# Performance work log

Measured on AMD Instinct MI355X. Metric: run time of the kernel, lower is better.

The kernel has to match this reference:

```python
import jax, jax.numpy as jnp
import numpy as np

EPS = 1e-5
DN = ('NCHW', 'OIHW', 'NCHW')


def ternarize(w):
    """Ternary Weight Network quantization with straight-through estimator.
    delta = 0.7 * mean|w|; alpha = mean of |w| over kept entries.
    """
    aw = jnp.abs(w)
    delta = 0.7 * aw.mean()
    mask = (aw > delta).astype(w.dtype)
    alpha = (aw * mask).sum() / jnp.maximum(mask.sum(), 1.0)
    q = alpha * jnp.sign(w) * mask
    return w + jax.lax.stop_gradient(q - w)


def bn(y, g, b, m, v):
    scale = (g / jnp.sqrt(v + EPS))[None, :, None, None]
    shift = (b - m * g / jnp.sqrt(v + EPS))[None, :, None, None]
    return y * scale + shift


def relu6(y):
    return jnp.clip(y, 0.0, 6.0)


def conv(x, w, stride=1, padding='VALID'):
    return jax.lax.conv_general_dilated(
        x, w, window_strides=(stride, stride), padding=padding,
        dimension_numbers=DN)


def setup_inputs() -> dict:
    key = jax.random.key(0)
    ks = jax.random.split(key, 16)
    inp, oup, expand = 32, 32, 6
    hidden = inp * expand  # 192
    B, H, W = 16, 112, 112
    d = {}
    d['x'] = jax.random.normal(ks[0], (B, inp, H, W), dtype=jnp.float32)
    # 1x1 expand conv
    d['w1'] = jax.random.normal(ks[1], (hidden, inp, 1, 1), dtype=jnp.float32) * 0.1
    d['g1'] = 1.0 + 0.1 * jax.random.normal(ks[2], (hidden,), dtype=jnp.float32)
    d['b1'] = 0.1 * jax.random.normal(ks[3], (hidden,), dtype=jnp.float32)
    d['m1'] = 0.1 * jax.random.normal(ks[4], (hidden,), dtype=jnp.float32)
    d['v1'] = jax.random.uniform(ks[5], (hidden,), minval=0.5, maxval=1.5, dtype=jnp.float32)
    # 3x3 dense conv (no groups in the source -> dense, not depthwise)
    d['w2'] = jax.random.normal(ks[6], (hidden, hidden, 3, 3), dtype=jnp.float32) * 0.05
    d['g2'] = 1.0 + 0.1 * jax.random.normal(ks[7], (hidden,), dtype=jnp.float32)
    d['b2'] = 0.1 * jax.random.normal(ks[8], (hidden,), dtype=jnp.float32)
    d['m2'] = 0.1 * jax.random.normal(ks[9], (hidden,), dtype=jnp.float32)
    d['v2'] = jax.random.uniform(ks[10], (hidden,), minval=0.5, maxval=1.5, dtype=jnp.float32)
    # 1x1 project conv
    d['w3'] = jax.random.normal(ks[11], (oup, hidden, 1, 1), dtype=jnp.float32) * 0.1
    d['g3'] = 1.0 + 0.1 * jax.random.normal(ks[12], (oup,), dtype=jnp.float32)
    d['b3'] = 0.1 * jax.random.normal(ks[13], (oup,), dtype=jnp.float32)
    d['m3'] = 0.1 * jax.random.normal(ks[14], (oup,), dtype=jnp.float32)
    d['v3'] = jax.random.uniform(ks[15], (oup,), minval=0.5, maxval=1.5, dtype=jnp.float32)
    return d


def reference(x, w1, g1, b1, m1, v1, w2, g2, b2, m2, v2, w3, g3, b3, m3, v3):
    # expand: 1x1 ternary conv -> BN -> ReLU6
    h = relu6(bn(conv(x, ternarize(w1)), g1, b1, m1, v1))
    # 3x3 ternary conv (stride=1, padding=1) -> BN -> ReLU6
    h = relu6(bn(conv(h, ternarize(w2), stride=1, padding=((1, 1), (1, 1))), g2, b2, m2, v2))
    # project: 1x1 ternary conv -> BN (no activation)
    h = bn(conv(h, ternarize(w3)), g3, b3, m3, v3)
    # residual connection (stride==1 and inp==oup)
    return x + h
```

## Files before the change

### kernel.cpp

```cpp
#include <hip/hip_runtime.h>


typedef __bf16 bf16x8 __attribute__((ext_vector_type(8)));
typedef __bf16 bf16x4 __attribute__((ext_vector_type(4)));
typedef float  f32x4  __attribute__((ext_vector_type(4)));

#define EPSBN 1e-5f

__device__ __forceinline__ void glds16(const void* g, void* l) {
  __builtin_amdgcn_global_load_lds(
      (const __attribute__((address_space(1))) void*)g,
      (__attribute__((address_space(3))) void*)l, 16, 0, 0);
}

__device__ __forceinline__ __bf16 tern(float w, float delta) {
  float aw = fabsf(w);
  float q = (aw > delta) ? ((w > 0.0f) ? 1.0f : -1.0f) : 0.0f;
  return (__bf16)q;
}


__global__ void stats_pass1(const float* __restrict__ w1, const float* __restrict__ w2,
                            const float* __restrict__ w3, double* __restrict__ pa) {
  __shared__ double red[256];
  int b = blockIdx.x, tid = threadIdx.x;
  int tix = b >> 5, slice = b & 31;
  const float* w = (tix == 0) ? w1 : (tix == 1) ? w2 : w3;
  int len = (tix == 1) ? 331776 : 6144;
  int per = len >> 5;
  int start = slice * per, end = start + per;
  double s = 0.0;
  for (int i = start + tid; i < end; i += 256) s += (double)fabsf(w[i]);
  red[tid] = s; __syncthreads();
  for (int off = 128; off > 0; off >>= 1) {
    if (tid < off) red[tid] += red[tid + off];
    __syncthreads();
  }
  if (tid == 0) pa[b] = red[0];
}

__global__ void stats_pass2(const float* __restrict__ w1, const float* __restrict__ w2,
                            const float* __restrict__ w3, const double* __restrict__ pa,
                            double* __restrict__ ps2, double* __restrict__ pc2) {
  __shared__ double red[256];
  int b = blockIdx.x, tid = threadIdx.x;
  int tix = b >> 5, slice = b & 31;
  const float* w = (tix == 0) ? w1 : (tix == 1) ? w2 : w3;
  int len = (tix == 1) ? 331776 : 6144;
  double tot = 0.0;
  for (int k = 0; k < 32; ++k) tot += pa[tix * 32 + k];
  float delta = 0.7f * (float)(tot / (double)len);
  int per = len >> 5;
  int start = slice * per, end = start + per;
  double s2 = 0.0, c2 = 0.0;
  for (int i = start + tid; i < end; i += 256) {
    float aw = fabsf(w[i]);
    if (aw > delta) { s2 += (double)aw; c2 += 1.0; }
  }
  red[tid] = s2; __syncthreads();
  for (int off = 128; off > 0; off >>= 1) {
    if (tid < off) red[tid] += red[tid + off];
    __syncthreads();
  }
  if (tid == 0) ps2[b] = red[0];
  __syncthreads();
  red[tid] = c2; __syncthreads();
  for (int off = 128; off > 0; off >>= 1) {
    if (tid < off) red[tid] += red[tid + off];
    __syncthreads();
  }
  if (tid == 0) pc2[b] = red[0];
}

__global__ void stats_pass3(const double* __restrict__ pa, const double* __restrict__ ps2,
                            const double* __restrict__ pc2, float* __restrict__ stats) {
  int tix = blockIdx.x;
  if (threadIdx.x != 0) return;
  double tot = 0.0, s2 = 0.0, c2 = 0.0;
  for (int k = 0; k < 32; ++k) {
    tot += pa[tix * 32 + k];
    s2  += ps2[tix * 32 + k];
    c2  += pc2[tix * 32 + k];
  }
  int len = (tix == 1) ? 331776 : 6144;
  stats[tix * 2]     = 0.7f * (float)(tot / (double)len);
  stats[tix * 2 + 1] = (float)(s2 / fmax(c2, 1.0));
}

__global__ void pack_kernel(
    const float* __restrict__ w1, const float* __restrict__ w2, const float* __restrict__ w3,
    const float* __restrict__ g1, const float* __restrict__ b1, const float* __restrict__ m1, const float* __restrict__ v1,
    const float* __restrict__ g2, const float* __restrict__ b2, const float* __restrict__ m2, const float* __restrict__ v2,
    const float* __restrict__ g3, const float* __restrict__ b3, const float* __restrict__ m3, const float* __restrict__ v3,
    const float* __restrict__ stats,
    __bf16* __restrict__ w1p, __bf16* __restrict__ w2p, __bf16* __restrict__ w3p,
    float* __restrict__ sc1, float* __restrict__ sh1,
    float* __restrict__ sc2, float* __restrict__ sh2,
    float* __restrict__ sc3, float* __restrict__ sh3) {
  int idx = blockIdx.x * 256 + threadIdx.x;
  if (idx < 331776) {
    float delta2 = stats[2];
    int c = idx / 6144, rem = idx - c * 6144;
    int co = rem >> 5, r5 = rem & 31;
    int cp = r5 >> 3, lo = r5 & 7;
    int tap = c / 6, cb = c - tap * 6;
    int ci = ((cp ^ ((co >> 2) & 3)) << 3) | lo;
    int cifull = cb * 32 + ci;
    w2p[idx] = tern(w2[(co * 192 + cifull) * 9 + tap], delta2);
    return;
  }
  idx -= 331776;
  if (idx < 6144) {
    int co = idx >> 5, c = (idx >> 3) & 3, lo = idx & 7;
    int ci = ((c ^ ((co >> 2) & 3)) << 3) | lo;
    w1p[idx] = tern(w1[co * 32 + ci], stats[0]);
    return;
  }
  idx -= 6144;
  if (idx < 6144) {
    int kc = idx >> 11, rem = idx & 2047;
    int co = rem >> 6, c = (rem >> 3) & 7, lo = rem & 7;
    int ci = ((c ^ (co & 7)) << 3) | lo;
    w3p[idx] = tern(w3[co * 192 + kc * 64 + ci], stats[4]);
    return;
  }
  idx -= 6144;
  if (idx < 192) {
    float rs = rsqrtf(v1[idx] + EPSBN);
    sc1[idx] = g1[idx] * rs * stats[1];
    sh1[idx] = b1[idx] - m1[idx] * g1[idx] * rs;
    return;
  }
  idx -= 192;
  if (idx < 192) {
    float rs = rsqrtf(v2[idx] + EPSBN);
    sc2[idx] = g2[idx] * rs * stats[3];
    sh2[idx] = b2[idx] - m2[idx] * g2[idx] * rs;
    return;
  }
  idx -= 192;
  if (idx < 32) {
    float rs = rsqrtf(v3[idx] + EPSBN);
    sc3[idx] = g3[idx] * rs * stats[5];
    sh3[idx] = b3[idx] - m3[idx] * g3[idx] * rs;
  }
}

__global__ __launch_bounds__(256)
void conv1_kernel(const float* __restrict__ x, const __bf16* __restrict__ w1p,
                  const float* __restrict__ scale1, const float* __restrict__ shift1,
                  __bf16* __restrict__ h1p) {
  __shared__ __bf16 smA[112 * 32];
  __shared__ __bf16 smB[192 * 32];
  int tid = threadIdx.x, lane = tid & 63, wave = tid >> 6;
  int h = blockIdx.x, n = blockIdx.y;

  for (int t = wave; t < 12; t += 4)
    glds16((const char*)w1p + t * 1024 + lane * 16, (char*)smB + t * 1024);

  const float* xrow = x + (long)n * 401408 + h * 112;
  for (int i = 0; i < 14; ++i) {
    int f = i * 256 + tid;
    int ci = f / 112, w = f - ci * 112;
    int col = ((ci >> 3) ^ ((w >> 2) & 3));
    smA[w * 32 + (col << 3) + (ci & 7)] = (__bf16)xrow[ci * 12544 + w];
  }
  __syncthreads();

  int mrow = lane & 15, quad = lane >> 4;
  int col16 = (quad ^ ((mrow >> 2) & 3)) * 16;
  int c0 = wave * 48;

  bf16x8 aw[3], bv[7];
#pragma unroll
  for (int ic = 0; ic < 3; ++ic)
    aw[ic] = *(const bf16x8*)((const char*)smB + (c0 + ic * 16 + mrow) * 64 + col16);
#pragma unroll
  for (int jp = 0; jp < 7; ++jp)
    bv[jp] = *(const bf16x8*)((const char*)smA + (jp * 16 + mrow) * 64 + col16);

  f32x4 acc[7][3];
#pragma unroll
  for (int jp = 0; jp < 7; ++jp)
#pragma unroll
    for (int ic = 0; ic < 3; ++ic) acc[jp][ic] = (f32x4)0.0f;

#pragma unroll
  for (int jp = 0; jp < 7; ++jp)
#pragma unroll
    for (int ic = 0; ic < 3; ++ic)
      acc[jp][ic] = __builtin_amdgcn_mfma_f32_16x16x32_bf16(aw[ic], bv[jp], acc[jp][ic], 0, 0, 0);

  __bf16* obase = h1p + ((long)(n * 114 + h + 1) * 114 + 1) * 192;
#pragma unroll
  for (int ic = 0; ic < 3; ++ic) {
    int co0 = c0 + ic * 16 + quad * 4;
    float4 sc = *(const float4*)(scale1 + co0);
    float4 sh = *(const float4*)(shift1 + co0);
#pragma unroll
    for (int jp = 0; jp < 7; ++jp) {
      int w = jp * 16 + mrow;
      bf16x4 o;
      o[0] = (__bf16)fminf(fmaxf(acc[jp][ic][0] * sc.x + sh.x, 0.0f), 6.0f);
      o[1] = (__bf16)fminf(fmaxf(acc[jp][ic][1] * sc.y + sh.y, 0.0f), 6.0f);
      o[2] = (__bf16)fminf(fmaxf(acc[jp][ic][2] * sc.z + sh.z, 0.0f), 6.0f);
      o[3] = (__bf16)fminf(fmaxf(acc[jp][ic][3] * sc.w + sh.w, 0.0f), 6.0f);
      *(bf16x4*)(obase + w * 192 + co0) = o;
    }
  }

  float4 z = make_float4(0.f, 0.f, 0.f, 0.f);
  if (tid < 48) {
    int px = (tid < 24) ? 0 : 113;
    int c8 = (tid < 24) ? tid : tid - 24;
    *(float4*)((char*)h1p + ((long)((n * 114 + h + 1) * 114 + px) * 384) + c8 * 16) = z;
  }
  if (h == 0) {
    for (int c = tid; c < 2736; c += 256)
      *(float4*)((char*)h1p + (long)(n * 114) * 114 * 384 + c * 16) = z;
  }
  if (h == 111) {
    for (int c = tid; c < 2736; c += 256)
      *(float4*)((char*)h1p + (long)(n * 114 + 113) * 114 * 384 + c * 16) = z;
  }
}

__global__ __launch_bounds__(256, 2)
void conv2_kernel(const __bf16* __restrict__ h1p, const __bf16* __restrict__ w2p,
                  const float* __restrict__ scale2, const float* __restrict__ shift2,
                  __bf16* __restrict__ h2) {
  __shared__ __bf16 smA[456 * 32];
  __shared__ __bf16 smB[2 * 192 * 32];
  int tid = threadIdx.x, lane = tid & 63, wave = tid >> 6;
  int bh = blockIdx.x, n = blockIdx.y;
  int h0 = bh * 2;

  int aoff[8];
#pragma unroll
  for (int it = 0; it < 8; ++it) {
    int t = wave + it * 4;
    int s = t * 64 + lane;
    if (s < 1824) {
      int q = s >> 2, c = s & 3;
      int q_log = c ^ ((q >> 2) & 3);
      int prow = q / 114, pcol = q - prow * 114;
      aoff[it] = ((n * 114 + h0 + prow) * 114 + pcol) * 384 + q_log * 16;
    } else {
      aoff[it] = -1;
    }
  }

  int pg = wave >> 1, cg = wave & 1;
  int mrow = lane & 15, quad = lane >> 4;
  int col16 = (quad ^ ((mrow >> 2) & 3)) * 16;
  const char* h1b = (const char*)h1p;
  const char* w2b = (const char*)w2p;

  f32x4 acc[7][6];
#pragma unroll
  for (int jp = 0; jp < 7; ++jp)
#pragma unroll
    for (int ic = 0; ic < 6; ++ic) acc[jp][ic] = (f32x4)0.0f;

  for (int cb = 0; cb < 6; ++cb) {
#pragma unroll
    for (int it = 0; it < 8; ++it) {
      int t = wave + it * 4;
      if (aoff[it] >= 0)
        glds16(h1b + aoff[it] + cb * 64, (char*)smA + t * 1024);
    }
#pragma unroll
    for (int it = 0; it < 3; ++it) {
      int t = wave + it * 4;
      glds16(w2b + (long)cb * 12288 + t * 1024 + lane * 16, (char*)smB + t * 1024);
    }
    __syncthreads();

    for (int tap = 0; tap < 9; ++tap) {
      int cur = tap & 1;
      if (tap < 8) {
#pragma unroll
        for (int it = 0; it < 3; ++it) {
          int t = wave + it * 4;
          glds16(w2b + (long)((tap + 1) * 6 + cb) * 12288 + t * 1024 + lane * 16,
                 (char*)smB + (cur ^ 1) * 12288 + t * 1024);
        }
      }
      int dy = tap / 3, dx = tap - dy * 3;
      const char* bbuf = (const char*)smB + cur * 12288;
      bf16x8 aw[6];
#pragma unroll
      for (int ic = 0; ic < 6; ++ic)
        aw[ic] = *(const bf16x8*)(bbuf + (cg * 96 + ic * 16 + mrow) * 64 + col16);
      int base = (pg + dy) * 114 + dx;
#pragma unroll
      for (int jp = 0; jp < 7; ++jp) {
        int row = base + jp * 16 + mrow;
        bf16x8 av = *(const bf16x8*)((const char*)smA + row * 64 +
                                     ((quad ^ ((row >> 2) & 3)) * 16));
#pragma unroll
        for (int ic = 0; ic < 6; ++ic)
          acc[jp][ic] = __builtin_amdgcn_mfma_f32_16x16x32_bf16(aw[ic], av, acc[jp][ic], 0, 0, 0);
      }
      __syncthreads();
    }
  }

  int h = h0 + pg;
  __bf16* orow = h2 + (long)((n * 112 + h) * 112) * 192;
#pragma unroll
  for (int ic = 0; ic < 6; ++ic) {
    int co0 = cg * 96 + ic * 16 + quad * 4;
    float4 sc = *(const float4*)(scale2 + co0);
    float4 sh = *(const float4*)(shift2 + co0);
#pragma unroll
    for (int jp = 0; jp < 7; ++jp) {
      int w = jp * 16 + mrow;
      bf16x4 o;
      o[0] = (__bf16)fminf(fmaxf(acc[jp][ic][0] * sc.x + sh.x, 0.0f), 6.0f);
      o[1] = (__bf16)fminf(fmaxf(acc[jp][ic][1] * sc.y + sh.y, 0.0f), 6.0f);
      o[2] = (__bf16)fminf(fmaxf(acc[jp][ic][2] * sc.z + sh.z, 0.0f), 6.0f);
      o[3] = (__bf16)fminf(fmaxf(acc[jp][ic][3] * sc.w + sh.w, 0.0f), 6.0f);
      *(bf16x4*)(orow + w * 192 + co0) = o;
    }
  }
}

__global__ __launch_bounds__(128)
void conv3_kernel(const __bf16* __restrict__ h2, const __bf16* __restrict__ w3p,
                  const float* __restrict__ scale3, const float* __restrict__ shift3,
                  const float* __restrict__ x, float* __restrict__ out) {
  __shared__ __bf16 smA[112 * 64];
  __shared__ __bf16 smB[32 * 64];
  int tid = threadIdx.x, lane = tid & 63, wv = tid >> 6;
  int h = blockIdx.x, n = blockIdx.y;
  int mrow = lane & 15, quad = lane >> 4;
  int swz7 = mrow & 7;

  const char* h2b = (const char*)h2 + (long)((n * 112 + h) * 112) * 384;
  f32x4 acc[7];
#pragma unroll
  for (int i = 0; i < 7; ++i) acc[i] = (f32x4)0.0f;

  for (int kc = 0; kc < 3; ++kc) {
    for (int t = wv; t < 18; t += 2) {
      if (t < 14) {
        int slot = t * 64 + lane;
        int w = slot >> 3, s = slot & 7;
        glds16(h2b + w * 384 + kc * 128 + (s ^ (w & 7)) * 16, (char*)smA + t * 1024);
      } else {
        glds16((const char*)w3p + kc * 4096 + (t - 14) * 1024 + lane * 16,
               (char*)smB + (t - 14) * 1024);
      }
    }
    __syncthreads();
    bf16x8 a[7][2], b[2];
#pragma unroll
    for (int ks = 0; ks < 2; ++ks) {
      int col = ((ks * 4 + quad) ^ swz7) * 16;
      b[ks] = *(const bf16x8*)((const char*)smB + (wv * 16 + mrow) * 128 + col);
#pragma unroll
      for (int i = 0; i < 7; ++i)
        a[i][ks] = *(const bf16x8*)((const char*)smA + (i * 16 + mrow) * 128 + col);
    }
    __syncthreads();
#pragma unroll
    for (int ks = 0; ks < 2; ++ks)
#pragma unroll
      for (int i = 0; i < 7; ++i)
        acc[i] = __builtin_amdgcn_mfma_f32_16x16x32_bf16(a[i][ks], b[ks], acc[i], 0, 0, 0);
  }

  int co = wv * 16 + mrow;
  float sc = scale3[co], sh = shift3[co];
  long obase = ((long)(n * 32 + co) * 112 + h) * 112;
  const float* xb = x + obase;
  float* ob = out + obase;
#pragma unroll
  for (int i = 0; i < 7; ++i) {
    int w0 = i * 16 + quad * 4;
    float4 xv = *(const float4*)(xb + w0);
    float4 o;
    o.x = acc[i][0] * sc + sh + xv.x;
    o.y = acc[i][1] * sc + sh + xv.y;
    o.z = acc[i][2] * sc + sh + xv.z;
    o.w = acc[i][3] * sc + sh + xv.w;
    *(float4*)(ob + w0) = o;
  }
}

extern "C" void kernel_launch(void* const* d_in, const int* in_sizes, int n_in,
                              void* d_out, int out_size, void* d_ws, size_t ws_size,
                              hipStream_t stream) {
  const float* x  = (const float*)d_in[0];
  const float* w1 = (const float*)d_in[1];
  const float* g1 = (const float*)d_in[2];
  const float* b1 = (const float*)d_in[3];
  const float* m1 = (const float*)d_in[4];
  const float* v1 = (const float*)d_in[5];
  const float* w2 = (const float*)d_in[6];
  const float* g2 = (const float*)d_in[7];
  const float* b2 = (const float*)d_in[8];
  const float* m2 = (const float*)d_in[9];
  const float* v2 = (const float*)d_in[10];
  const float* w3 = (const float*)d_in[11];
  const float* g3 = (const float*)d_in[12];
  const float* b3 = (const float*)d_in[13];
  const float* m3 = (const float*)d_in[14];
  const float* v3 = (const float*)d_in[15];
  float* out = (float*)d_out;

  char* ws = (char*)d_ws;
  float*  stats = (float*)ws;
  double* pa    = (double*)(ws + 256);
  double* ps2   = (double*)(ws + 1024);
  double* pc2   = (double*)(ws + 1792);
  float* sc1 = (float*)(ws + 2560);
  float* sh1 = (float*)(ws + 3328);
  float* sc2 = (float*)(ws + 4096);
  float* sh2 = (float*)(ws + 4864);
  float* sc3 = (float*)(ws + 5632);
  float* sh3 = (float*)(ws + 5760);
  __bf16* w1p = (__bf16*)(ws + 8192);
  __bf16* w3p = (__bf16*)(ws + 20480);
  __bf16* w2p = (__bf16*)(ws + 32768);
  __bf16* h1p = (__bf16*)(ws + (1 << 20));
  __bf16* h2  = (__bf16*)(ws + (1 << 20) + 79847424);

  hipLaunchKernelGGL(stats_pass1, dim3(96), dim3(256), 0, stream, w1, w2, w3, pa);
  hipLaunchKernelGGL(stats_pass2, dim3(96), dim3(256), 0, stream, w1, w2, w3, pa, ps2, pc2);
  hipLaunchKernelGGL(stats_pass3, dim3(3), dim3(64), 0, stream, pa, ps2, pc2, stats);
  hipLaunchKernelGGL(pack_kernel, dim3(1346), dim3(256), 0, stream, w1, w2, w3,
                     g1, b1, m1, v1, g2, b2, m2, v2, g3, b3, m3, v3, stats,
                     w1p, w2p, w3p, sc1, sh1, sc2, sh2, sc3, sh3);
  hipLaunchKernelGGL(conv1_kernel, dim3(112, 16), dim3(256), 0, stream, x, w1p, sc1, sh1, h1p);
  hipLaunchKernelGGL(conv2_kernel, dim3(56, 16), dim3(256), 0, stream, h1p, w2p, sc2, sh2, h2);
  hipLaunchKernelGGL(conv3_kernel, dim3(112, 16), dim3(128), 0, stream, h2, w3p, sc3, sh3, x, out);
}
```

Measured before the change: 299.7 us.

## Deepen conv2 weight prefetch to four LDS buffers with fine-grained vmcnt waits

The 3x3 conv kernel now keeps four weight buffers in LDS and prefetches two taps ahead, replacing full __syncthreads with explicit vmcnt waits plus raw barriers. The next channel block's activation and first two weight tiles are issued right after the last tap instead of at the top of the loop. s_setprio is raised around the MFMA block. The aim is to hide global-to-LDS load latency behind MFMA work. The cost is extra LDS, which may reduce occupancy, and a dependence on hand-counted vmcnt values being correct.

```diff
diff --git a/kernel.cpp b/kernel.cpp
--- a/kernel.cpp
+++ b/kernel.cpp
@@ -225,12 +225,29 @@
   }
 }
 
+
+#define STAGE_W(TAP, CB, B) do {                                              \
+  _Pragma("unroll")                                                           \
+  for (int it_ = 0; it_ < 3; ++it_) {                                         \
+    int t_ = wave + it_ * 4;                                                  \
+    glds16(w2b + (long)((TAP) * 6 + (CB)) * 12288 + t_ * 1024 + lane * 16,    \
+           (char*)smB + (B) * 12288 + t_ * 1024);                             \
+  }                                                                           \
+} while (0)
+
+#define STAGE_A(CB) do {                                                      \
+  _Pragma("unroll")                                                           \
+  for (int it_ = 0; it_ < 8; ++it_)                                           \
+    if (aoff[it_] >= 0)                                                       \
+      glds16(h1b + aoff[it_] + (CB) * 64, (char*)smA + (wave + it_ * 4) * 1024); \
+} while (0)
+
 __global__ __launch_bounds__(256, 2)
 void conv2_kernel(const __bf16* __restrict__ h1p, const __bf16* __restrict__ w2p,
                   const float* __restrict__ scale2, const float* __restrict__ shift2,
                   __bf16* __restrict__ h2) {
   __shared__ __bf16 smA[456 * 32];
-  __shared__ __bf16 smB[2 * 192 * 32];
+  __shared__ __bf16 smB[4 * 192 * 32];
   int tid = threadIdx.x, lane = tid & 63, wave = tid >> 6;
   int bh = blockIdx.x, n = blockIdx.y;
   int h0 = bh * 2;
@@ -262,37 +279,33 @@
 #pragma unroll
     for (int ic = 0; ic < 6; ++ic) acc[jp][ic] = (f32x4)0.0f;
 
+  STAGE_A(0);
+  STAGE_W(0, 0, 0);
+  STAGE_W(1, 0, 1);
+
   for (int cb = 0; cb < 6; ++cb) {
 #pragma unroll
-    for (int it = 0; it < 8; ++it) {
-      int t = wave + it * 4;
-      if (aoff[it] >= 0)
-        glds16(h1b + aoff[it] + cb * 64, (char*)smA + t * 1024);
-    }
-#pragma unroll
-    for (int it = 0; it < 3; ++it) {
-      int t = wave + it * 4;
-      glds16(w2b + (long)cb * 12288 + t * 1024 + lane * 16, (char*)smB + t * 1024);
-    }
-    __syncthreads();
-
     for (int tap = 0; tap < 9; ++tap) {
-      int cur = tap & 1;
-      if (tap < 8) {
-#pragma unroll
-        for (int it = 0; it < 3; ++it) {
-          int t = wave + it * 4;
-          glds16(w2b + (long)((tap + 1) * 6 + cb) * 12288 + t * 1024 + lane * 16,
-                 (char*)smB + (cur ^ 1) * 12288 + t * 1024);
-        }
+      if (tap <= 6) {
+        STAGE_W(tap + 2, cb, (tap + 2) & 3);
+        asm volatile("s_waitcnt vmcnt(6)" ::: "memory");
+      } else if (tap == 7) {
+        asm volatile("s_waitcnt vmcnt(3)" ::: "memory");
+      } else {
+        asm volatile("s_waitcnt vmcnt(0)" ::: "memory");
       }
-      int dy = tap / 3, dx = tap - dy * 3;
-      const char* bbuf = (const char*)smB + cur * 12288;
+      __builtin_amdgcn_s_barrier();
+      __builtin_amdgcn_sched_barrier(0);
+
+      const char* bbuf = (const char*)smB + (tap & 3) * 12288;
       bf16x8 aw[6];
 #pragma unroll
       for (int ic = 0; ic < 6; ++ic)
         aw[ic] = *(const bf16x8*)(bbuf + (cg * 96 + ic * 16 + mrow) * 64 + col16);
+
+      int dy = tap / 3, dx = tap - dy * 3;
       int base = (pg + dy) * 114 + dx;
+      __builtin_amdgcn_s_setprio(1);
 #pragma unroll
       for (int jp = 0; jp < 7; ++jp) {
         int row = base + jp * 16 + mrow;
@@ -302,7 +315,16 @@
         for (int ic = 0; ic < 6; ++ic)
           acc[jp][ic] = __builtin_amdgcn_mfma_f32_16x16x32_bf16(aw[ic], av, acc[jp][ic], 0, 0, 0);
       }
-      __syncthreads();
+      __builtin_amdgcn_s_setprio(0);
+    }
+
+    if (cb < 5) {
+      asm volatile("s_waitcnt lgkmcnt(0)" ::: "memory");
+      __builtin_amdgcn_sched_barrier(0);
+      __builtin_amdgcn_s_barrier();
+      STAGE_A(cb + 1);
+      STAGE_W(0, cb + 1, 0);
+      STAGE_W(1, cb + 1, 1);
     }
   }
 
```

Result: no change. 295.6 us (-1.4%).
